# Kernel optimization log

Hardware: AMD Instinct MI355X
Metric: run time of the kernel (lower is better)

The kernel has to match this reference:

```python
import jax, jax.numpy as jnp
import numpy as np

B, C, H, W = 2, 512, 64, 64
G = 32  # GroupNorm groups
EPS = 1e-6


def setup_inputs() -> dict:
    key = jax.random.key(0)
    ks = jax.random.split(key, 6)
    s = 1.0 / np.sqrt(C)
    return {
        "x": jax.random.normal(ks[0], (B, C, H, W), dtype=jnp.float32),
        "gn_w": jnp.ones((C,), dtype=jnp.float32),
        "gn_b": jnp.zeros((C,), dtype=jnp.float32),
        "wq": jax.random.normal(ks[1], (C, C), dtype=jnp.float32) * s,
        "bq": jnp.zeros((C,), dtype=jnp.float32),
        "wk": jax.random.normal(ks[2], (C, C), dtype=jnp.float32) * s,
        "bk": jnp.zeros((C,), dtype=jnp.float32),
        "wv": jax.random.normal(ks[3], (C, C), dtype=jnp.float32) * s,
        "bv": jnp.zeros((C,), dtype=jnp.float32),
        "wo": jax.random.normal(ks[4], (C, C), dtype=jnp.float32) * s,
        "bo": jnp.zeros((C,), dtype=jnp.float32),
    }


def _group_norm(x, w, b):
    b_, c_, h_, w_ = x.shape
    xg = x.reshape(b_, G, c_ // G, h_ * w_)
    mu = jnp.mean(xg, axis=(2, 3), keepdims=True)
    var = jnp.var(xg, axis=(2, 3), keepdims=True)
    xn = (xg - mu) * jax.lax.rsqrt(var + EPS)
    xn = xn.reshape(b_, c_, h_ * w_)
    return xn * w[None, :, None] + b[None, :, None]  # [B, C, N]


def reference(x, gn_w, gn_b, wq, bq, wk, bk, wv, bv, wo, bo):
    b, c, h, w = x.shape
    hn = _group_norm(x, gn_w, gn_b)  # [B, C, N]
    # 1x1 convs == per-pixel matmuls over channel dim
    q = jnp.einsum('oc,bcn->bon', wq, hn) + bq[None, :, None]
    k = jnp.einsum('oc,bcn->bon', wk, hn) + bk[None, :, None]
    v = jnp.einsum('oc,bcn->bon', wv, hn) + bv[None, :, None]
    scale = jnp.asarray(c, x.dtype) ** -0.5
    attn = jnp.einsum('bci,bcj->bij', q, k) * scale  # [B, N, N]
    attn = jax.nn.softmax(attn, axis=-1)
    o = jnp.einsum('bij,bcj->bci', attn, v)  # [B, C, N]
    o = jnp.einsum('oc,bcn->bon', wo, o) + bo[None, :, None]
    return x + o.reshape(b, c, h, w)
```

## Files before the change

### kernel.cpp

```cpp
#include <hip/hip_runtime.h>

#define CC 512
#define NPIX 4096
#define NB 2
#define NG 32
#define GSIZE 16
#define EPS 1e-6f

typedef unsigned short u16;
typedef __bf16 bf16x8 __attribute__((ext_vector_type(8)));
typedef float f32x4 __attribute__((ext_vector_type(4)));

__device__ __forceinline__ float bf2f(u16 u) {
  union { unsigned int i; float f; } c; c.i = ((unsigned int)u) << 16; return c.f;
}
__device__ __forceinline__ u16 f2bf(float f) {
  union { float f; unsigned int i; } c; c.f = f;
  unsigned int u = c.i;
  return (u16)((u + 0x7fffu + ((u >> 16) & 1u)) >> 16);
}

__global__ __launch_bounds__(256) void f2bf4x4_kernel(
    const float* __restrict__ s0, const float* __restrict__ s1,
    const float* __restrict__ s2, const float* __restrict__ s3,
    u16* __restrict__ d0, u16* __restrict__ d1,
    u16* __restrict__ d2, u16* __restrict__ d3) {
  const float* s; u16* d;
  switch (blockIdx.y) {
    case 0: s = s0; d = d0; break;
    case 1: s = s1; d = d1; break;
    case 2: s = s2; d = d2; break;
    default: s = s3; d = d3; break;
  }
  int i = blockIdx.x * 256 + threadIdx.x;
  float4 v = ((const float4*)s)[i];
  uint2 pk;
  pk.x = (unsigned)f2bf(v.x) | ((unsigned)f2bf(v.y) << 16);
  pk.y = (unsigned)f2bf(v.z) | ((unsigned)f2bf(v.w) << 16);
  ((uint2*)d)[i] = pk;
}

__global__ __launch_bounds__(256) void concat2_kernel(const float* __restrict__ a,
                                                      const float* __restrict__ b,
                                                      float* __restrict__ o) {
  int i = blockIdx.x * 256 + threadIdx.x;
  o[i] = (i < CC) ? a[i] : b[i - CC];
}

__global__ __launch_bounds__(256) void gn_stats_kernel(const float* __restrict__ x,
                                                       float* __restrict__ stats) {
  int bg = blockIdx.x;
  const float4* p = (const float4*)(x + (long)bg * (GSIZE * NPIX));
  float s = 0.f, ss = 0.f;
  for (int i = threadIdx.x; i < GSIZE * NPIX / 4; i += 256) {
    float4 v = p[i];
    s  += v.x + v.y + v.z + v.w;
    ss += v.x * v.x + v.y * v.y + v.z * v.z + v.w * v.w;
  }
  for (int off = 32; off; off >>= 1) { s += __shfl_xor(s, off); ss += __shfl_xor(ss, off); }
  __shared__ float rs[4], rss[4];
  int wid = threadIdx.x >> 6;
  if ((threadIdx.x & 63) == 0) { rs[wid] = s; rss[wid] = ss; }
  __syncthreads();
  if (threadIdx.x == 0) {
    s = rs[0] + rs[1] + rs[2] + rs[3];
    ss = rss[0] + rss[1] + rss[2] + rss[3];
    float mean = s / (float)(GSIZE * NPIX);
    float var = ss / (float)(GSIZE * NPIX) - mean * mean;
    stats[bg * 2] = mean;
    stats[bg * 2 + 1] = rsqrtf(var + EPS);
  }
}

__global__ __launch_bounds__(256) void gn_apply_kernel(const float* __restrict__ x,
                                                       const float* __restrict__ stats,
                                                       const float* __restrict__ gw,
                                                       const float* __restrict__ gb,
                                                       u16* __restrict__ hn) {
  int n0 = blockIdx.x * 64, c0 = blockIdx.y * 64, b = blockIdx.z;
  __shared__ float tile[64][65];
  int t = threadIdx.x;
  int nj = t & 63, cw = t >> 6;
  #pragma unroll
  for (int r = 0; r < 16; ++r) {
    int ci = cw * 16 + r;
    int c = c0 + ci;
    float mean = stats[(b * NG + (c >> 4)) * 2];
    float rstd = stats[(b * NG + (c >> 4)) * 2 + 1];
    float v = x[((long)b * CC + c) * NPIX + n0 + nj];
    tile[ci][nj] = (v - mean) * rstd * gw[c] + gb[c];
  }
  __syncthreads();
  #pragma unroll
  for (int r = 0; r < 16; ++r) {
    int nn = cw * 16 + r;
    hn[((long)b * NPIX + n0 + nn) * CC + c0 + nj] = f2bf(tile[nj][nn]);
  }
}

#define BM 128
#define BN 128
#define BKT 64
#define BUFSZ 8192

template<int OUTF32, int BIASMODE, int RESID, int EPI>
__global__ __launch_bounds__(256) void gemm_nt(
    const u16* __restrict__ A, int lda, long aBatch,
    const u16* __restrict__ B, int ldb, long bBatch,
    void* __restrict__ C, int ldc, long cBatch,
    const float* __restrict__ bias,
    const float* __restrict__ resid, long rBatch,
    float* __restrict__ L, int lOff,
    int K, float scale) {
  __shared__ u16 SH[2 * 2 * BUFSZ];
  const int t = threadIdx.x;

  int nwgx = gridDim.x, nwgy = gridDim.y;
  int flat = blockIdx.x + nwgx * (blockIdx.y + nwgy * blockIdx.z);
  int nwg = nwgx * nwgy * gridDim.z;
  int newflat = (flat % 8) * (nwg / 8) + flat / 8;
  const int bx = newflat % nwgx;
  int tmpf = newflat / nwgx;
  const int by = tmpf % nwgy;
  const int bz = tmpf / nwgy;

  const int m0 = by * BM;
  const int n0 = bx * BN;
  const u16* Ab = A + (long)bz * aBatch;
  const u16* Bb = B + (long)bz * bBatch;

  const int lane = t & 63;
  const int wid = t >> 6;
  const int wr = (wid >> 1) * 64;
  const int wc = (wid & 1) * 64;
  const int r16 = lane & 15;
  const int q = lane >> 4;

  const int sRow = wid * 8 + (lane >> 3);
  const int sCol = (((lane & 7) ^ (lane >> 3)) * 8);

  f32x4 acc[4][4] = {};
  const int rsw = r16 & 7;

  const int nt = K / BKT;

  auto stage = [&](int c, int k0) {
    u16* aDst = SH + c * 2 * BUFSZ + wid * 512;
    u16* bDst = SH + c * 2 * BUFSZ + BUFSZ + wid * 512;
    #pragma unroll
    for (int p = 0; p < 4; ++p) {
      __builtin_amdgcn_global_load_lds(
          (const __attribute__((address_space(1))) unsigned int*)(Ab + (long)(m0 + p * 32 + sRow) * lda + k0 + sCol),
          (__attribute__((address_space(3))) unsigned int*)(aDst + p * 2048),
          16, 0, 0);
      __builtin_amdgcn_global_load_lds(
          (const __attribute__((address_space(1))) unsigned int*)(Bb + (long)(n0 + p * 32 + sRow) * ldb + k0 + sCol),
          (__attribute__((address_space(3))) unsigned int*)(bDst + p * 2048),
          16, 0, 0);
    }
  };

  stage(0, 0);

  for (int tt = 0; tt < nt; ++tt) {
    const int pre = tt + 1;
    if (pre < nt) {
      stage(pre & 1, pre * BKT);
      asm volatile("s_waitcnt vmcnt(8)" ::: "memory");
    } else {
      asm volatile("s_waitcnt vmcnt(0)" ::: "memory");
    }
    __builtin_amdgcn_s_barrier();
    __builtin_amdgcn_sched_barrier(0);

    const u16* As_b = SH + (tt & 1) * 2 * BUFSZ;
    const u16* Bs_b = As_b + BUFSZ;
    #pragma unroll
    for (int kk = 0; kk < BKT; kk += 32) {
      bf16x8 af[4], bfr[4];
      const int c0q = (kk >> 3) + q;
      const int colSw = (c0q ^ rsw) * 8;
      #pragma unroll
      for (int i = 0; i < 4; ++i) {
        af[i]  = *(const bf16x8*)&As_b[(wr + i * 16 + r16) * BKT + colSw];
        bfr[i] = *(const bf16x8*)&Bs_b[(wc + i * 16 + r16) * BKT + colSw];
      }
      #pragma unroll
      for (int i = 0; i < 4; ++i)
        #pragma unroll
        for (int j = 0; j < 4; ++j)
          acc[i][j] = __builtin_amdgcn_mfma_f32_16x16x32_bf16(af[i], bfr[j], acc[i][j], 0, 0, 0);
    }
    __builtin_amdgcn_s_barrier();
    __builtin_amdgcn_sched_barrier(0);
  }

  if (EPI == 1) {
    #pragma unroll
    for (int i = 0; i < 4; ++i) {
      #pragma unroll
      for (int r = 0; r < 4; ++r) {
        int row = m0 + wr + i * 16 + q * 4 + r;
        float s = 0.f;
        #pragma unroll
        for (int j = 0; j < 4; ++j) {
          float p = __expf(acc[i][j][r] * scale);
          s += p;
          int col = n0 + wc + j * 16 + r16;
          ((u16*)C)[(long)bz * cBatch + (long)row * ldc + col] = f2bf(p);
        }
        s += __shfl_xor(s, 1); s += __shfl_xor(s, 2);
        s += __shfl_xor(s, 4); s += __shfl_xor(s, 8);
        if (r16 == 0) atomicAdd(&L[(long)bz * NPIX + lOff + row], s);
      }
    }
    return;
  }

  #pragma unroll
  for (int i = 0; i < 4; ++i) {
    #pragma unroll
    for (int r = 0; r < 4; ++r) {
      int row = m0 + wr + i * 16 + q * 4 + r;
      float inv = 1.0f;
      if (EPI == 2) inv = 1.0f / L[(long)bz * NPIX + lOff + row];
      #pragma unroll
      for (int j = 0; j < 4; ++j) {
        int col = n0 + wc + j * 16 + r16;
        float v = acc[i][j][r] * scale;
        if (EPI == 2) v *= inv;
        if (BIASMODE == 1) v += bias[row];
        if (BIASMODE == 2) v += bias[col];
        long off = (long)bz * cBatch + (long)row * ldc + col;
        if (RESID) v += resid[(long)bz * rBatch + (long)row * ldc + col];
        if (OUTF32) ((float*)C)[off] = v;
        else        ((u16*)C)[off] = f2bf(v);
      }
    }
  }
}

__global__ __launch_bounds__(512, 2) void gemm256_exp(
    const u16* __restrict__ A, int lda, long aBatch,
    const u16* __restrict__ B, int ldb, long bBatch,
    u16* __restrict__ C, int ldc, long cBatch,
    float* __restrict__ L,
    int K, float scale) {
  __shared__ u16 SH[2][32768];
  const int t = threadIdx.x;

  int nwgx = gridDim.x, nwgy = gridDim.y;
  int flat = blockIdx.x + nwgx * (blockIdx.y + nwgy * blockIdx.z);
  int nwg = nwgx * nwgy * gridDim.z;
  int newflat = (flat % 8) * (nwg / 8) + flat / 8;
  const int bx = newflat % nwgx;
  int tmpf = newflat / nwgx;
  const int by = tmpf % nwgy;
  const int bz = tmpf / nwgy;

  const int m0 = by * 256;
  const int n0 = bx * 256;
  const u16* Ab = A + (long)bz * aBatch;
  const u16* Bb = B + (long)bz * bBatch;
  u16* Cb = C + (long)bz * cBatch;

  const int lane = t & 63;
  const int wid = t >> 6;
  const int wrow = (wid >> 2) * 128;
  const int wcol = (wid & 3) * 64;
  const int r16 = lane & 15;
  const int q = lane >> 4;
  const int rsw = r16 & 7;

  const int sRow = t >> 3;
  const int sCol = ((t & 7) ^ ((t >> 3) & 7)) * 8;

  auto stage = [&](int d, int k0) {
    u16* base = &SH[d][0];
    #pragma unroll
    for (int i = 0; i < 4; ++i)
      __builtin_amdgcn_global_load_lds(
          (const __attribute__((address_space(1))) unsigned int*)(Ab + (long)(m0 + i * 64 + sRow) * lda + k0 + sCol),
          (__attribute__((address_space(3))) unsigned int*)(base + i * 4096 + wid * 512),
          16, 0, 0);
    #pragma unroll
    for (int i = 0; i < 4; ++i)
      __builtin_amdgcn_global_load_lds(
          (const __attribute__((address_space(1))) unsigned int*)(Bb + (long)(n0 + i * 64 + sRow) * ldb + k0 + sCol),
          (__attribute__((address_space(3))) unsigned int*)(base + 16384 + i * 4096 + wid * 512),
          16, 0, 0);
  };

  f32x4 acc[8][4] = {};
  const int nt = K / 64;

  stage(0, 0);

  for (int tt = 0; tt < nt; ++tt) {
    const u16* As_ = &SH[tt & 1][0];
    const u16* Bs_ = As_ + 16384;
    if (tt + 1 < nt) {
      stage((tt + 1) & 1, (tt + 1) * 64);
      asm volatile("s_waitcnt vmcnt(8)" ::: "memory");
    } else {
      asm volatile("s_waitcnt vmcnt(0)" ::: "memory");
    }
    __builtin_amdgcn_s_barrier();
    __builtin_amdgcn_sched_barrier(0);

    bf16x8 a0[4], a1[4], b0[4], b1[4];
    const int c0 = (q ^ rsw) * 8;
    const int c1 = ((4 + q) ^ rsw) * 8;

    #pragma unroll
    for (int i = 0; i < 4; ++i)
      a0[i] = *(const bf16x8*)&As_[(wrow + i * 16 + r16) * 64 + c0];
    #pragma unroll
    for (int i = 0; i < 4; ++i)
      b0[i] = *(const bf16x8*)&Bs_[(wcol + i * 16 + r16) * 64 + c0];
    asm volatile("s_waitcnt lgkmcnt(0)" ::: "memory");
    __builtin_amdgcn_sched_barrier(0);
    __builtin_amdgcn_s_setprio(1);
    #pragma unroll
    for (int mi = 0; mi < 4; ++mi)
      #pragma unroll
      for (int ni = 0; ni < 4; ++ni)
        acc[mi][ni] = __builtin_amdgcn_mfma_f32_16x16x32_bf16(a0[mi], b0[ni], acc[mi][ni], 0, 0, 0);
    __builtin_amdgcn_s_setprio(0);
    __builtin_amdgcn_s_barrier();

    #pragma unroll
    for (int i = 0; i < 4; ++i)
      a1[i] = *(const bf16x8*)&As_[(wrow + (4 + i) * 16 + r16) * 64 + c0];
    asm volatile("s_waitcnt lgkmcnt(0)" ::: "memory");
    __builtin_amdgcn_sched_barrier(0);
    __builtin_amdgcn_s_setprio(1);
    #pragma unroll
    for (int mi = 0; mi < 4; ++mi)
      #pragma unroll
      for (int ni = 0; ni < 4; ++ni)
        acc[4 + mi][ni] = __builtin_amdgcn_mfma_f32_16x16x32_bf16(a1[mi], b0[ni], acc[4 + mi][ni], 0, 0, 0);
    __builtin_amdgcn_s_setprio(0);
    __builtin_amdgcn_s_barrier();

    #pragma unroll
    for (int i = 0; i < 4; ++i)
      a0[i] = *(const bf16x8*)&As_[(wrow + i * 16 + r16) * 64 + c1];
    #pragma unroll
    for (int i = 0; i < 4; ++i)
      b1[i] = *(const bf16x8*)&Bs_[(wcol + i * 16 + r16) * 64 + c1];
    asm volatile("s_waitcnt lgkmcnt(0)" ::: "memory");
    __builtin_amdgcn_sched_barrier(0);
    __builtin_amdgcn_s_setprio(1);
    #pragma unroll
    for (int mi = 0; mi < 4; ++mi)
      #pragma unroll
      for (int ni = 0; ni < 4; ++ni)
        acc[mi][ni] = __builtin_amdgcn_mfma_f32_16x16x32_bf16(a0[mi], b1[ni], acc[mi][ni], 0, 0, 0);
    __builtin_amdgcn_s_setprio(0);
    __builtin_amdgcn_s_barrier();

    #pragma unroll
    for (int i = 0; i < 4; ++i)
      a1[i] = *(const bf16x8*)&As_[(wrow + (4 + i) * 16 + r16) * 64 + c1];
    asm volatile("s_waitcnt lgkmcnt(0)" ::: "memory");
    __builtin_amdgcn_sched_barrier(0);
    __builtin_amdgcn_s_setprio(1);
    #pragma unroll
    for (int mi = 0; mi < 4; ++mi)
      #pragma unroll
      for (int ni = 0; ni < 4; ++ni)
        acc[4 + mi][ni] = __builtin_amdgcn_mfma_f32_16x16x32_bf16(a1[mi], b1[ni], acc[4 + mi][ni], 0, 0, 0);
    __builtin_amdgcn_s_setprio(0);
    __builtin_amdgcn_s_barrier();
    __builtin_amdgcn_sched_barrier(0);
  }

  u16* Ps = &SH[0][0];
  #pragma unroll
  for (int mi = 0; mi < 8; ++mi) {
    #pragma unroll
    for (int r = 0; r < 4; ++r) {
      int lrow = wrow + mi * 16 + q * 4 + r;
      float s = 0.f;
      #pragma unroll
      for (int ni = 0; ni < 4; ++ni) {
        float p = __expf(acc[mi][ni][r] * scale);
        s += p;
        Ps[lrow * 256 + wcol + ni * 16 + r16] = f2bf(p);
      }
      s += __shfl_xor(s, 1); s += __shfl_xor(s, 2);
      s += __shfl_xor(s, 4); s += __shfl_xor(s, 8);
      if (r16 == 0) atomicAdd(&L[(long)bz * NPIX + m0 + lrow], s);
    }
  }
  __syncthreads();
  {
    const int rr = t >> 5;
    const int c8 = (t & 31) * 8;
    #pragma unroll
    for (int pp = 0; pp < 16; ++pp) {
      int lrow = pp * 16 + rr;
      uint4 v = *(const uint4*)&Ps[lrow * 256 + c8];
      *(uint4*)&Cb[(long)(m0 + lrow) * ldc + n0 + c8] = v;
    }
  }
}

extern "C" void kernel_launch(void* const* d_in, const int* in_sizes, int n_in,
                              void* d_out, int out_size, void* d_ws, size_t ws_size,
                              hipStream_t stream) {
  const float* x   = (const float*)d_in[0];
  const float* gnw = (const float*)d_in[1];
  const float* gnb = (const float*)d_in[2];
  const float* wq  = (const float*)d_in[3];
  const float* bq  = (const float*)d_in[4];
  const float* wk  = (const float*)d_in[5];
  const float* bk_ = (const float*)d_in[6];
  const float* wv  = (const float*)d_in[7];
  const float* bv  = (const float*)d_in[8];
  const float* wo  = (const float*)d_in[9];
  const float* bo  = (const float*)d_in[10];
  float* out = (float*)d_out;

  char* wsp = (char*)d_ws;
  auto alloc = [&](size_t bytes) {
    char* r = wsp; wsp += (bytes + 255) & ~(size_t)255; return r;
  };
  u16* wqb = (u16*)alloc((size_t)CC * CC * 2);
  u16* wkb = (u16*)alloc((size_t)CC * CC * 2);
  u16* wvb = (u16*)alloc((size_t)CC * CC * 2);
  u16* wob = (u16*)alloc((size_t)CC * CC * 2);
  float* bqk = (float*)alloc((size_t)2 * CC * 4);
  float* stats = (float*)alloc((size_t)NB * NG * 2 * 4);
  float* lsum = (float*)alloc((size_t)NB * NPIX * 4);
  u16* hn  = (u16*)alloc((size_t)NB * NPIX * CC * 2);
  u16* qkt = (u16*)alloc((size_t)NB * NPIX * (2 * CC) * 2);
  u16* vcn = (u16*)alloc((size_t)NB * CC * NPIX * 2);
  u16* ot  = (u16*)alloc((size_t)NB * NPIX * CC * 2);
  size_t used = (size_t)(wsp - (char*)d_ws);
  size_t rem = ws_size > used ? ws_size - used : 0;
  int CH = 256;
  if ((size_t)NB * 1024 * NPIX * 2 <= rem) CH = 1024;
  if ((size_t)NB * 4096 * NPIX * 2 <= rem) CH = 4096;
  u16* SP = (u16*)alloc((size_t)NB * CH * NPIX * 2);

  dim3 blk(256);
  f2bf4x4_kernel<<<dim3(CC * CC / 1024, 4), blk, 0, stream>>>(
      wq, wk, wv, wo, wqb, wkb, wvb, wob);
  concat2_kernel<<<2 * CC / 256, blk, 0, stream>>>(bq, bk_, bqk);
  hipMemsetAsync(lsum, 0, (size_t)NB * NPIX * 4, stream);

  gn_stats_kernel<<<NB * NG, blk, 0, stream>>>(x, stats);
  gn_apply_kernel<<<dim3(NPIX / 64, CC / 64, NB), blk, 0, stream>>>(x, stats, gnw, gnb, hn);

  gemm_nt<0, 2, 0, 0><<<dim3(2 * CC / BN, NPIX / BM, NB), blk, 0, stream>>>(
      hn, CC, (long)NPIX * CC, wqb, CC, 0, qkt, 2 * CC, (long)NPIX * 2 * CC,
      bqk, nullptr, 0, nullptr, 0, CC, 1.0f);
  gemm_nt<0, 1, 0, 0><<<dim3(NPIX / BN, CC / BM, NB), blk, 0, stream>>>(
      wvb, CC, 0, hn, CC, (long)NPIX * CC, vcn, NPIX, (long)CC * NPIX,
      bv, nullptr, 0, nullptr, 0, CC, 1.0f);

  const u16* qt = qkt;
  const u16* kt = qkt + CC;
  const float scale = 0.044194173824159216f;
  for (int i0 = 0; i0 < NPIX; i0 += CH) {
    if (CH == 4096) {
      gemm256_exp<<<dim3(NPIX / 256, NPIX / 256, NB), dim3(512), 0, stream>>>(
          qt, 2 * CC, (long)NPIX * 2 * CC, kt, 2 * CC, (long)NPIX * 2 * CC,
          SP, NPIX, (long)CH * NPIX, lsum, CC, scale);
    } else {
      gemm_nt<0, 0, 0, 1><<<dim3(NPIX / BN, CH / BM, NB), blk, 0, stream>>>(
          qt + (long)i0 * 2 * CC, 2 * CC, (long)NPIX * 2 * CC, kt, 2 * CC, (long)NPIX * 2 * CC,
          SP, NPIX, (long)CH * NPIX, nullptr, nullptr, 0, lsum, i0, CC, scale);
    }
    gemm_nt<0, 0, 0, 2><<<dim3(CC / BN, CH / BM, NB), blk, 0, stream>>>(
        SP, NPIX, (long)CH * NPIX, vcn, NPIX, (long)CC * NPIX,
        ot + (long)i0 * CC, CC, (long)NPIX * CC, nullptr, nullptr, 0, lsum, i0, NPIX, 1.0f);
  }

  gemm_nt<1, 1, 1, 0><<<dim3(NPIX / BN, CC / BM, NB), blk, 0, stream>>>(
      wob, CC, 0, ot, CC, (long)NPIX * CC, out, NPIX, (long)CC * NPIX,
      bo, x, (long)CC * NPIX, nullptr, 0, CC, 1.0f);
}
```

Baseline: 184.0 us.

## Simplify QK^T exp GEMM main loop and write P directly to global

Replaces the hand-scheduled four-phase LDS-read/MFMA loop, with its sched_barriers, setprio and intermediate barriers, by a plain two-step k-loop that loads all A and B fragments and lets the compiler schedule. The epilogue now writes exp scores straight to global memory with 2-byte scattered stores instead of staging through LDS for coalesced 16-byte stores. Launch bounds drop from 2 to 1 waves-per-EU occupancy hint. The intent is presumably fewer barriers and more register freedom, at the cost of lost explicit interleaving and less coalesced output stores.

```diff
diff --git a/kernel.cpp b/kernel.cpp
--- a/kernel.cpp
+++ b/kernel.cpp
@@ -240,7 +240,7 @@
   }
 }
 
-__global__ __launch_bounds__(512, 2) void gemm256_exp(
+__global__ __launch_bounds__(512, 1) void gemm256_exp(
     const u16* __restrict__ A, int lda, long aBatch,
     const u16* __restrict__ B, int ldb, long bBatch,
     u16* __restrict__ C, int ldc, long cBatch,
@@ -297,8 +297,6 @@
   stage(0, 0);
 
   for (int tt = 0; tt < nt; ++tt) {
-    const u16* As_ = &SH[tt & 1][0];
-    const u16* Bs_ = As_ + 16384;
     if (tt + 1 < nt) {
       stage((tt + 1) & 1, (tt + 1) * 64);
       asm volatile("s_waitcnt vmcnt(8)" ::: "memory");
@@ -306,103 +304,43 @@
       asm volatile("s_waitcnt vmcnt(0)" ::: "memory");
     }
     __builtin_amdgcn_s_barrier();
-    __builtin_amdgcn_sched_barrier(0);
-
-    bf16x8 a0[4], a1[4], b0[4], b1[4];
-    const int c0 = (q ^ rsw) * 8;
-    const int c1 = ((4 + q) ^ rsw) * 8;
-
-    #pragma unroll
-    for (int i = 0; i < 4; ++i)
-      a0[i] = *(const bf16x8*)&As_[(wrow + i * 16 + r16) * 64 + c0];
-    #pragma unroll
-    for (int i = 0; i < 4; ++i)
-      b0[i] = *(const bf16x8*)&Bs_[(wcol + i * 16 + r16) * 64 + c0];
-    asm volatile("s_waitcnt lgkmcnt(0)" ::: "memory");
-    __builtin_amdgcn_sched_barrier(0);
-    __builtin_amdgcn_s_setprio(1);
-    #pragma unroll
-    for (int mi = 0; mi < 4; ++mi)
-      #pragma unroll
-      for (int ni = 0; ni < 4; ++ni)
-        acc[mi][ni] = __builtin_amdgcn_mfma_f32_16x16x32_bf16(a0[mi], b0[ni], acc[mi][ni], 0, 0, 0);
-    __builtin_amdgcn_s_setprio(0);
+
+    const u16* As_ = &SH[tt & 1][0];
+    const u16* Bs_ = As_ + 16384;
+    #pragma unroll
+    for (int kk = 0; kk < 2; ++kk) {
+      const int cs = ((kk * 4 + q) ^ rsw) * 8;
+      bf16x8 af[8], bfv[4];
+      #pragma unroll
+      for (int i = 0; i < 8; ++i)
+        af[i] = *(const bf16x8*)&As_[(wrow + i * 16 + r16) * 64 + cs];
+      #pragma unroll
+      for (int i = 0; i < 4; ++i)
+        bfv[i] = *(const bf16x8*)&Bs_[(wcol + i * 16 + r16) * 64 + cs];
+      #pragma unroll
+      for (int mi = 0; mi < 8; ++mi)
+        #pragma unroll
+        for (int ni = 0; ni < 4; ++ni)
+          acc[mi][ni] = __builtin_amdgcn_mfma_f32_16x16x32_bf16(af[mi], bfv[ni], acc[mi][ni], 0, 0, 0);
+    }
     __builtin_amdgcn_s_barrier();
-
-    #pragma unroll
-    for (int i = 0; i < 4; ++i)
-      a1[i] = *(const bf16x8*)&As_[(wrow + (4 + i) * 16 + r16) * 64 + c0];
-    asm volatile("s_waitcnt lgkmcnt(0)" ::: "memory");
-    __builtin_amdgcn_sched_barrier(0);
-    __builtin_amdgcn_s_setprio(1);
-    #pragma unroll
-    for (int mi = 0; mi < 4; ++mi)
-      #pragma unroll
-      for (int ni = 0; ni < 4; ++ni)
-        acc[4 + mi][ni] = __builtin_amdgcn_mfma_f32_16x16x32_bf16(a1[mi], b0[ni], acc[4 + mi][ni], 0, 0, 0);
-    __builtin_amdgcn_s_setprio(0);
-    __builtin_amdgcn_s_barrier();
-
-    #pragma unroll
-    for (int i = 0; i < 4; ++i)
-      a0[i] = *(const bf16x8*)&As_[(wrow + i * 16 + r16) * 64 + c1];
-    #pragma unroll
-    for (int i = 0; i < 4; ++i)
-      b1[i] = *(const bf16x8*)&Bs_[(wcol + i * 16 + r16) * 64 + c1];
-    asm volatile("s_waitcnt lgkmcnt(0)" ::: "memory");
-    __builtin_amdgcn_sched_barrier(0);
-    __builtin_amdgcn_s_setprio(1);
-    #pragma unroll
-    for (int mi = 0; mi < 4; ++mi)
-      #pragma unroll
-      for (int ni = 0; ni < 4; ++ni)
-        acc[mi][ni] = __builtin_amdgcn_mfma_f32_16x16x32_bf16(a0[mi], b1[ni], acc[mi][ni], 0, 0, 0);
-    __builtin_amdgcn_s_setprio(0);
-    __builtin_amdgcn_s_barrier();
-
-    #pragma unroll
-    for (int i = 0; i < 4; ++i)
-      a1[i] = *(const bf16x8*)&As_[(wrow + (4 + i) * 16 + r16) * 64 + c1];
-    asm volatile("s_waitcnt lgkmcnt(0)" ::: "memory");
-    __builtin_amdgcn_sched_barrier(0);
-    __builtin_amdgcn_s_setprio(1);
-    #pragma unroll
-    for (int mi = 0; mi < 4; ++mi)
-      #pragma unroll
-      for (int ni = 0; ni < 4; ++ni)
-        acc[4 + mi][ni] = __builtin_amdgcn_mfma_f32_16x16x32_bf16(a1[mi], b1[ni], acc[4 + mi][ni], 0, 0, 0);
-    __builtin_amdgcn_s_setprio(0);
-    __builtin_amdgcn_s_barrier();
-    __builtin_amdgcn_sched_barrier(0);
-  }
-
-  u16* Ps = &SH[0][0];
+  }
+
   #pragma unroll
   for (int mi = 0; mi < 8; ++mi) {
     #pragma unroll
     for (int r = 0; r < 4; ++r) {
-      int lrow = wrow + mi * 16 + q * 4 + r;
+      int row = m0 + wrow + mi * 16 + q * 4 + r;
       float s = 0.f;
       #pragma unroll
       for (int ni = 0; ni < 4; ++ni) {
         float p = __expf(acc[mi][ni][r] * scale);
         s += p;
-        Ps[lrow * 256 + wcol + ni * 16 + r16] = f2bf(p);
+        Cb[(long)row * ldc + n0 + wcol + ni * 16 + r16] = f2bf(p);
       }
       s += __shfl_xor(s, 1); s += __shfl_xor(s, 2);
       s += __shfl_xor(s, 4); s += __shfl_xor(s, 8);
-      if (r16 == 0) atomicAdd(&L[(long)bz * NPIX + m0 + lrow], s);
-    }
-  }
-  __syncthreads();
-  {
-    const int rr = t >> 5;
-    const int c8 = (t & 31) * 8;
-    #pragma unroll
-    for (int pp = 0; pp < 16; ++pp) {
-      int lrow = pp * 16 + rr;
-      uint4 v = *(const uint4*)&Ps[lrow * 256 + c8];
-      *(uint4*)&Cb[(long)(m0 + lrow) * ldc + n0 + c8] = v;
+      if (r16 == 0) atomicAdd(&L[(long)bz * NPIX + row], s);
     }
   }
 }
```

Result: no change. 181.4 us (-1.4%).
